# Optimization experiments

Hardware: AMD Instinct MI355X
Metric: run time of the kernel (lower is better)

The kernel has to match this reference:

```python
import jax, jax.numpy as jnp
import numpy as np

D_MODEL = 1024
NUM_EXPERTS = 64
TOP_K = 2
TEMPERATURE = 1.0


def setup_inputs() -> dict:
    key = jax.random.key(0)
    k1, k2, k3, k4 = jax.random.split(key, 4)
    mh_output = jax.random.normal(k1, (8, 4096, D_MODEL), dtype=jnp.float32)
    noise = jax.random.normal(k2, (8, 4096, NUM_EXPERTS), dtype=jnp.float32)  # randn_like sample, externalized
    # nn.Linear weights: shape [out, in], init normal(0, 0.02); biases zero
    W_route = jax.random.normal(k3, (NUM_EXPERTS, D_MODEL), dtype=jnp.float32) * 0.02
    b_route = jnp.zeros((NUM_EXPERTS,), dtype=jnp.float32)
    W_noise = jax.random.normal(k4, (NUM_EXPERTS, D_MODEL), dtype=jnp.float32) * 0.02
    b_noise = jnp.zeros((NUM_EXPERTS,), dtype=jnp.float32)
    return {"mh_output": mh_output, "noise": noise, "W_route": W_route,
            "b_route": b_route, "W_noise": W_noise, "b_noise": b_noise}


def reference(mh_output, noise, W_route, b_route, W_noise, b_noise):
    # logits = topkroute_linear(mh_output); noise_logits = noise_linear(mh_output)
    logits = jnp.einsum('bsd,ed->bse', mh_output, W_route) + b_route
    noise_logits = jnp.einsum('bsd,ed->bse', mh_output, W_noise) + b_noise
    # noisy logits = logits + temperature * randn * softplus(noise_logits)
    noisy = logits + TEMPERATURE * noise * jax.nn.softplus(noise_logits)
    # top-k, scatter into -inf, softmax  ==  softmax over top-k values scattered into zeros
    top_vals, indices = jax.lax.top_k(noisy, TOP_K)          # [b, s, k]
    probs_k = jax.nn.softmax(top_vals, axis=-1)              # softmax(-inf elsewhere) -> 0 elsewhere
    one_hot = jax.nn.one_hot(indices, NUM_EXPERTS, dtype=noisy.dtype)  # [b, s, k, E]
    router_output = jnp.sum(one_hot * probs_k[..., None], axis=-2)     # [b, s, E]
    return router_output, indices
```

## Files before the change

kernel.cpp:

```cpp
#include <hip/hip_runtime.h>
#include <math.h>


#define T_TOKENS 32768
#define D_MODEL  1024
#define NE       64
#define NCOL     128
#define M_TILE   32
#define NCHUNK   (D_MODEL / 32)
#define CS_LD    68
#define OUT_IDX_BASE ((size_t)T_TOKENS * NE)
#define W_ELEMS  (NCOL * D_MODEL)

typedef short  bf16x8  __attribute__((ext_vector_type(8)));
typedef float  floatx4 __attribute__((ext_vector_type(4)));

__device__ __forceinline__ unsigned short f32_to_bf16_rne(float x) {
    unsigned u = __float_as_uint(x);
    unsigned r = u + 0x7fffu + ((u >> 16) & 1u);
    return (unsigned short)(r >> 16);
}
__device__ __forceinline__ float bf16_bits_to_f32(unsigned short h) {
    return __uint_as_float(((unsigned)h) << 16);
}
__device__ __forceinline__ float softplus_f(float x) {
    return fmaxf(x, 0.f) + log1pf(expf(-fabsf(x)));
}

__global__ __launch_bounds__(256) void prepack_w(
    const float* __restrict__ Wr, const float* __restrict__ Wn,
    short* __restrict__ Bh, short* __restrict__ Bl)
{
    int g   = blockIdx.x * 256 + threadIdx.x;
    int n   = g & 15;
    int kg  = (g >> 4) & 127;
    int t2  = g >> 11;
    int col = t2 * 16 + n;
    const float* src = (col < NE ? Wr + (size_t)col * D_MODEL
                                 : Wn + (size_t)(col - NE) * D_MODEL) + kg * 8;
    float4 a = *(const float4*)src;
    float4 b = *(const float4*)(src + 4);
    float v[8] = {a.x, a.y, a.z, a.w, b.x, b.y, b.z, b.w};
    unsigned short h[8], l[8];
    #pragma unroll
    for (int j = 0; j < 8; ++j) {
        h[j] = f32_to_bf16_rne(v[j]);
        l[j] = f32_to_bf16_rne(v[j] - bf16_bits_to_f32(h[j]));
    }
    int4 hp, lp;
    hp.x = (int)((unsigned)h[0] | ((unsigned)h[1] << 16));
    hp.y = (int)((unsigned)h[2] | ((unsigned)h[3] << 16));
    hp.z = (int)((unsigned)h[4] | ((unsigned)h[5] << 16));
    hp.w = (int)((unsigned)h[6] | ((unsigned)h[7] << 16));
    lp.x = (int)((unsigned)l[0] | ((unsigned)l[1] << 16));
    lp.y = (int)((unsigned)l[2] | ((unsigned)l[3] << 16));
    lp.z = (int)((unsigned)l[4] | ((unsigned)l[5] << 16));
    lp.w = (int)((unsigned)l[6] | ((unsigned)l[7] << 16));
    *(int4*)(Bh + (size_t)g * 8) = hp;
    *(int4*)(Bl + (size_t)g * 8) = lp;
}

__global__ __launch_bounds__(256, 4) void router_mfma(
    const float* __restrict__ A,
    const float* __restrict__ noise,
    const float* __restrict__ br,
    const float* __restrict__ bn,
    const short* __restrict__ Bh,
    const short* __restrict__ Bl,
    float* __restrict__ out)
{
    __shared__ __align__(16) short Ah[2][M_TILE * 32];
    __shared__ __align__(16) short Al[2][M_TILE * 32];
    __shared__ float Cs[M_TILE * CS_LD];
    __shared__ float s_p1[M_TILE], s_p2[M_TILE];
    __shared__ int   s_e1[M_TILE], s_e2[M_TILE];

    const int tid  = threadIdx.x;
    const int lane = tid & 63;
    const int wid  = tid >> 6;
    const int n16  = lane & 15;
    const int quad = lane >> 4;
    const int m0   = blockIdx.x * M_TILE;

    const int ms = tid >> 3;
    const int kq = tid & 7;
    const float* pA = A + (size_t)(m0 + ms) * D_MODEL + kq * 4;
    const int sBase = ((kq >> 1) * M_TILE + ms) * 8 + (kq & 1) * 4;

    const int bBaseR = ((wid * 128 + quad) * 16 + n16) * 8;
    const int bBaseN = (((4 + wid) * 128 + quad) * 16 + n16) * 8;

    floatx4 acc[2][2];
    #pragma unroll
    for (int i = 0; i < 2; ++i) { acc[i][0] = (floatx4)0.f; acc[i][1] = (floatx4)0.f; }

#define CONVERT_STORE(buf_, f4_) do {                                       \
        float v_[4] = {(f4_).x, (f4_).y, (f4_).z, (f4_).w};                  \
        unsigned short h_[4], l_[4];                                         \
        _Pragma("unroll")                                                    \
        for (int j_ = 0; j_ < 4; ++j_) {                                     \
            h_[j_] = f32_to_bf16_rne(v_[j_]);                                \
            l_[j_] = f32_to_bf16_rne(v_[j_] - bf16_bits_to_f32(h_[j_]));     \
        }                                                                    \
        int2 hp_, lp_;                                                       \
        hp_.x = (int)((unsigned)h_[0] | ((unsigned)h_[1] << 16));            \
        hp_.y = (int)((unsigned)h_[2] | ((unsigned)h_[3] << 16));            \
        lp_.x = (int)((unsigned)l_[0] | ((unsigned)l_[1] << 16));            \
        lp_.y = (int)((unsigned)l_[2] | ((unsigned)l_[3] << 16));            \
        *(int2*)&Ah[(buf_)][sBase] = hp_;                                    \
        *(int2*)&Al[(buf_)][sBase] = lp_;                                    \
    } while (0)

    {
        float4 a0 = *(const float4*)pA;
        CONVERT_STORE(0, a0);
    }
    bf16x8 bhR, blR, bhN, blN;
    bhR = *(const bf16x8*)(Bh + bBaseR);
    blR = *(const bf16x8*)(Bl + bBaseR);
    bhN = *(const bf16x8*)(Bh + bBaseN);
    blN = *(const bf16x8*)(Bl + bBaseN);
    float4 aP1 = *(const float4*)(pA + 32);
    __syncthreads();

    for (int kc = 0; kc < NCHUNK; ++kc) {
        const int cur = kc & 1, nxt = cur ^ 1;

        float4 aP2;
        if (kc + 2 < NCHUNK)
            aP2 = *(const float4*)(pA + (kc + 2) * 32);

        bf16x8 bhRn, blRn, bhNn, blNn;
        if (kc + 1 < NCHUNK) {
            int o = (kc + 1) * 512;
            bhRn = *(const bf16x8*)(Bh + bBaseR + o);
            blRn = *(const bf16x8*)(Bl + bBaseR + o);
            bhNn = *(const bf16x8*)(Bh + bBaseN + o);
            blNn = *(const bf16x8*)(Bl + bBaseN + o);
        }

        bf16x8 afh[2], afl[2];
        #pragma unroll
        for (int mf = 0; mf < 2; ++mf) {
            int g = (quad * M_TILE + mf * 16 + n16) * 8;
            afh[mf] = *(const bf16x8*)&Ah[cur][g];
            afl[mf] = *(const bf16x8*)&Al[cur][g];
        }

        #pragma unroll
        for (int mf = 0; mf < 2; ++mf) {
            acc[mf][0] = __builtin_amdgcn_mfma_f32_16x16x32_bf16(afh[mf], bhR, acc[mf][0], 0, 0, 0);
            acc[mf][0] = __builtin_amdgcn_mfma_f32_16x16x32_bf16(afh[mf], blR, acc[mf][0], 0, 0, 0);
            acc[mf][0] = __builtin_amdgcn_mfma_f32_16x16x32_bf16(afl[mf], bhR, acc[mf][0], 0, 0, 0);
            acc[mf][1] = __builtin_amdgcn_mfma_f32_16x16x32_bf16(afh[mf], bhN, acc[mf][1], 0, 0, 0);
            acc[mf][1] = __builtin_amdgcn_mfma_f32_16x16x32_bf16(afh[mf], blN, acc[mf][1], 0, 0, 0);
            acc[mf][1] = __builtin_amdgcn_mfma_f32_16x16x32_bf16(afl[mf], bhN, acc[mf][1], 0, 0, 0);
        }

        if (kc + 1 < NCHUNK)
            CONVERT_STORE(nxt, aP1);

        __syncthreads();

        aP1 = aP2;
        bhR = bhRn; blR = blRn; bhN = bhNn; blN = blNn;
    }

    {
        int e = wid * 16 + n16;
        float brv = br[e], bnv = bn[e];
        #pragma unroll
        for (int mf = 0; mf < 2; ++mf)
            #pragma unroll
            for (int r = 0; r < 4; ++r) {
                int t = mf * 16 + quad * 4 + r;
                float nz    = noise[(size_t)(m0 + t) * NE + e];
                float route = acc[mf][0][r] + brv;
                float nl    = acc[mf][1][r] + bnv;
                Cs[t * CS_LD + e] = fmaf(nz, softplus_f(nl), route);
            }
    }
    __syncthreads();

    if (tid < M_TILE) {
        const int t = tid;
        float v1 = -INFINITY, v2 = -INFINITY;
        int e1 = 0, e2 = 0;
        #pragma unroll 8
        for (int e = 0; e < NE; ++e) {
            float v = Cs[t * CS_LD + e];
            if (v > v1) { v2 = v1; e2 = e1; v1 = v; e1 = e; }
            else if (v > v2) { v2 = v; e2 = e; }
        }
        float ex = expf(v2 - v1);
        float denom = 1.f + ex;
        s_p1[t] = 1.f / denom;
        s_p2[t] = ex / denom;
        s_e1[t] = e1;
        s_e2[t] = e2;
        float2 iv = make_float2((float)e1, (float)e2);
        *(float2*)(out + OUT_IDX_BASE + (size_t)(m0 + t) * 2) = iv;
    }
    __syncthreads();

    #pragma unroll
    for (int i = 0; i < 2; ++i) {
        int gi = i * 256 + tid;
        int t  = gi >> 4;
        int e0 = (gi & 15) * 4;
        float p1 = s_p1[t], p2 = s_p2[t];
        int   e1 = s_e1[t], e2 = s_e2[t];
        float4 v;
        v.x = (e0 + 0 == e1) ? p1 : ((e0 + 0 == e2) ? p2 : 0.f);
        v.y = (e0 + 1 == e1) ? p1 : ((e0 + 1 == e2) ? p2 : 0.f);
        v.z = (e0 + 2 == e1) ? p1 : ((e0 + 2 == e2) ? p2 : 0.f);
        v.w = (e0 + 3 == e1) ? p1 : ((e0 + 3 == e2) ? p2 : 0.f);
        *(float4*)(out + (size_t)(m0 + t) * NE + e0) = v;
    }
}

extern "C" void kernel_launch(void* const* d_in, const int* in_sizes, int n_in,
                              void* d_out, int out_size, void* d_ws, size_t ws_size,
                              hipStream_t stream) {
    const float* A     = (const float*)d_in[0];
    const float* noise = (const float*)d_in[1];
    const float* Wr    = (const float*)d_in[2];
    const float* br    = (const float*)d_in[3];
    const float* Wn    = (const float*)d_in[4];
    const float* bn    = (const float*)d_in[5];
    float* out = (float*)d_out;

    short* Bh = (short*)d_ws;
    short* Bl = Bh + W_ELEMS;

    prepack_w<<<dim3(W_ELEMS / 8 / 256), dim3(256), 0, stream>>>(Wr, Wn, Bh, Bl);
    router_mfma<<<dim3(T_TOKENS / M_TILE), dim3(256), 0, stream>>>(A, noise, br, bn, Bh, Bl, out);
}
```

Baseline: 232.6 us.

## Double K-chunk per stage and deepen A register prefetch to three stages

Each loop iteration now processes 64 K elements (two 32-wide chunks) instead of 32, halving the number of __syncthreads barriers and doubling the LDS staging buffers. Activation prefetch into registers is deepened to three stages ahead. Weight fragments are no longer prefetched one iteration early; they are loaded at the top of the same iteration in which they are used. LDS stores for the next stage are moved before the MFMAs so they can overlap. The cost is higher register pressure and exposed B-load latency, which risks occupancy under launch_bounds(256,4).

```diff
diff --git a/kernel.cpp b/kernel.cpp
--- a/kernel.cpp
+++ b/kernel.cpp
@@ -7,7 +7,7 @@
 #define NE       64
 #define NCOL     128
 #define M_TILE   32
-#define NCHUNK   (D_MODEL / 32)
+#define NSTAGE   (D_MODEL / 64)
 #define CS_LD    68
 #define OUT_IDX_BASE ((size_t)T_TOKENS * NE)
 #define W_ELEMS  (NCOL * D_MODEL)
@@ -69,8 +69,8 @@
     const short* __restrict__ Bl,
     float* __restrict__ out)
 {
-    __shared__ __align__(16) short Ah[2][M_TILE * 32];
-    __shared__ __align__(16) short Al[2][M_TILE * 32];
+    __shared__ __align__(16) short Ah[2][2 * M_TILE * 32];
+    __shared__ __align__(16) short Al[2][2 * M_TILE * 32];
     __shared__ float Cs[M_TILE * CS_LD];
     __shared__ float s_p1[M_TILE], s_p2[M_TILE];
     __shared__ int   s_e1[M_TILE], s_e2[M_TILE];
@@ -94,7 +94,7 @@
     #pragma unroll
     for (int i = 0; i < 2; ++i) { acc[i][0] = (floatx4)0.f; acc[i][1] = (floatx4)0.f; }
 
-#define CONVERT_STORE(buf_, f4_) do {                                       \
+#define CONVERT_STORE(buf_, c_, f4_) do {                                    \
         float v_[4] = {(f4_).x, (f4_).y, (f4_).z, (f4_).w};                  \
         unsigned short h_[4], l_[4];                                         \
         _Pragma("unroll")                                                    \
@@ -107,63 +107,73 @@
         hp_.y = (int)((unsigned)h_[2] | ((unsigned)h_[3] << 16));            \
         lp_.x = (int)((unsigned)l_[0] | ((unsigned)l_[1] << 16));            \
         lp_.y = (int)((unsigned)l_[2] | ((unsigned)l_[3] << 16));            \
-        *(int2*)&Ah[(buf_)][sBase] = hp_;                                    \
-        *(int2*)&Al[(buf_)][sBase] = lp_;                                    \
+        *(int2*)&Ah[(buf_)][(c_) * (M_TILE * 32) + sBase] = hp_;             \
+        *(int2*)&Al[(buf_)][(c_) * (M_TILE * 32) + sBase] = lp_;             \
     } while (0)
 
     {
-        float4 a0 = *(const float4*)pA;
-        CONVERT_STORE(0, a0);
-    }
-    bf16x8 bhR, blR, bhN, blN;
-    bhR = *(const bf16x8*)(Bh + bBaseR);
-    blR = *(const bf16x8*)(Bl + bBaseR);
-    bhN = *(const bf16x8*)(Bh + bBaseN);
-    blN = *(const bf16x8*)(Bl + bBaseN);
-    float4 aP1 = *(const float4*)(pA + 32);
+        float4 s0c0 = *(const float4*)(pA);
+        float4 s0c1 = *(const float4*)(pA + 32);
+        CONVERT_STORE(0, 0, s0c0);
+        CONVERT_STORE(0, 1, s0c1);
+    }
+    float4 aP1[2], aP2[2];
+    aP1[0] = *(const float4*)(pA + 64);
+    aP1[1] = *(const float4*)(pA + 96);
+    aP2[0] = *(const float4*)(pA + 128);
+    aP2[1] = *(const float4*)(pA + 160);
     __syncthreads();
 
-    for (int kc = 0; kc < NCHUNK; ++kc) {
-        const int cur = kc & 1, nxt = cur ^ 1;
-
-        float4 aP2;
-        if (kc + 2 < NCHUNK)
-            aP2 = *(const float4*)(pA + (kc + 2) * 32);
-
-        bf16x8 bhRn, blRn, bhNn, blNn;
-        if (kc + 1 < NCHUNK) {
-            int o = (kc + 1) * 512;
-            bhRn = *(const bf16x8*)(Bh + bBaseR + o);
-            blRn = *(const bf16x8*)(Bl + bBaseR + o);
-            bhNn = *(const bf16x8*)(Bh + bBaseN + o);
-            blNn = *(const bf16x8*)(Bl + bBaseN + o);
-        }
-
-        bf16x8 afh[2], afl[2];
-        #pragma unroll
-        for (int mf = 0; mf < 2; ++mf) {
-            int g = (quad * M_TILE + mf * 16 + n16) * 8;
-            afh[mf] = *(const bf16x8*)&Ah[cur][g];
-            afl[mf] = *(const bf16x8*)&Al[cur][g];
-        }
-
-        #pragma unroll
-        for (int mf = 0; mf < 2; ++mf) {
-            acc[mf][0] = __builtin_amdgcn_mfma_f32_16x16x32_bf16(afh[mf], bhR, acc[mf][0], 0, 0, 0);
-            acc[mf][0] = __builtin_amdgcn_mfma_f32_16x16x32_bf16(afh[mf], blR, acc[mf][0], 0, 0, 0);
-            acc[mf][0] = __builtin_amdgcn_mfma_f32_16x16x32_bf16(afl[mf], bhR, acc[mf][0], 0, 0, 0);
-            acc[mf][1] = __builtin_amdgcn_mfma_f32_16x16x32_bf16(afh[mf], bhN, acc[mf][1], 0, 0, 0);
-            acc[mf][1] = __builtin_amdgcn_mfma_f32_16x16x32_bf16(afh[mf], blN, acc[mf][1], 0, 0, 0);
-            acc[mf][1] = __builtin_amdgcn_mfma_f32_16x16x32_bf16(afl[mf], bhN, acc[mf][1], 0, 0, 0);
-        }
-
-        if (kc + 1 < NCHUNK)
-            CONVERT_STORE(nxt, aP1);
+    for (int ks = 0; ks < NSTAGE; ++ks) {
+        const int cur = ks & 1, nxt = cur ^ 1;
+
+        bf16x8 bhR[2], blR[2], bhN[2], blN[2];
+        #pragma unroll
+        for (int c = 0; c < 2; ++c) {
+            int o = (2 * ks + c) * 512;
+            bhR[c] = *(const bf16x8*)(Bh + bBaseR + o);
+            blR[c] = *(const bf16x8*)(Bl + bBaseR + o);
+            bhN[c] = *(const bf16x8*)(Bh + bBaseN + o);
+            blN[c] = *(const bf16x8*)(Bl + bBaseN + o);
+        }
+
+        float4 aP3[2];
+        if (ks + 3 < NSTAGE) {
+            aP3[0] = *(const float4*)(pA + (ks + 3) * 64);
+            aP3[1] = *(const float4*)(pA + (ks + 3) * 64 + 32);
+        }
+
+        bf16x8 afh[2][2], afl[2][2];
+        #pragma unroll
+        for (int c = 0; c < 2; ++c)
+            #pragma unroll
+            for (int mf = 0; mf < 2; ++mf) {
+                int g = c * (M_TILE * 32) + (quad * M_TILE + mf * 16 + n16) * 8;
+                afh[c][mf] = *(const bf16x8*)&Ah[cur][g];
+                afl[c][mf] = *(const bf16x8*)&Al[cur][g];
+            }
+
+        if (ks + 1 < NSTAGE) {
+            CONVERT_STORE(nxt, 0, aP1[0]);
+            CONVERT_STORE(nxt, 1, aP1[1]);
+        }
+
+        #pragma unroll
+        for (int c = 0; c < 2; ++c)
+            #pragma unroll
+            for (int mf = 0; mf < 2; ++mf) {
+                acc[mf][0] = __builtin_amdgcn_mfma_f32_16x16x32_bf16(afh[c][mf], bhR[c], acc[mf][0], 0, 0, 0);
+                acc[mf][0] = __builtin_amdgcn_mfma_f32_16x16x32_bf16(afh[c][mf], blR[c], acc[mf][0], 0, 0, 0);
+                acc[mf][0] = __builtin_amdgcn_mfma_f32_16x16x32_bf16(afl[c][mf], bhR[c], acc[mf][0], 0, 0, 0);
+                acc[mf][1] = __builtin_amdgcn_mfma_f32_16x16x32_bf16(afh[c][mf], bhN[c], acc[mf][1], 0, 0, 0);
+                acc[mf][1] = __builtin_amdgcn_mfma_f32_16x16x32_bf16(afh[c][mf], blN[c], acc[mf][1], 0, 0, 0);
+                acc[mf][1] = __builtin_amdgcn_mfma_f32_16x16x32_bf16(afl[c][mf], bhN[c], acc[mf][1], 0, 0, 0);
+            }
 
         __syncthreads();
 
-        aP1 = aP2;
-        bhR = bhRn; blR = blRn; bhN = bhNn; blN = blNn;
+        aP1[0] = aP2[0]; aP1[1] = aP2[1];
+        aP2[0] = aP3[0]; aP2[1] = aP3[1];
     }
 
     {
```

After: 233.2 us. About the same (+0.3%).

## Double token tile to 64 and deepen A prefetch with packed bf16 split conversion

Applied to the files above, without the earlier changes.

Doubles the per-block token tile from 32 to 64 so each loaded weight fragment feeds twice as many MFMAs. This halves the weight traffic per token and the number of blocks. The A-tile loader now has each thread convert 8 floats with packed bf16x2 intrinsics, and prefetch is three chunks ahead. The conversion and LDS store move before the MFMAs, and the top-2 scan reads float4 vectors from shared memory. Launch bounds drop to 2 blocks per CU, which raises register use and reduces occupancy.

```diff
diff --git a/kernel.cpp b/kernel.cpp
--- a/kernel.cpp
+++ b/kernel.cpp
@@ -1,4 +1,5 @@
 #include <hip/hip_runtime.h>
+#include <hip/hip_bf16.h>
 #include <math.h>
 
 
@@ -6,8 +7,8 @@
 #define D_MODEL  1024
 #define NE       64
 #define NCOL     128
-#define M_TILE   32
-#define NCHUNK   (D_MODEL / 32)
+#define M_TILE   64
+#define NCHUNK   32
 #define CS_LD    68
 #define OUT_IDX_BASE ((size_t)T_TOKENS * NE)
 #define W_ELEMS  (NCOL * D_MODEL)
@@ -15,16 +16,28 @@
 typedef short  bf16x8  __attribute__((ext_vector_type(8)));
 typedef float  floatx4 __attribute__((ext_vector_type(4)));
 
-__device__ __forceinline__ unsigned short f32_to_bf16_rne(float x) {
-    unsigned u = __float_as_uint(x);
-    unsigned r = u + 0x7fffu + ((u >> 16) & 1u);
-    return (unsigned short)(r >> 16);
-}
-__device__ __forceinline__ float bf16_bits_to_f32(unsigned short h) {
-    return __uint_as_float(((unsigned)h) << 16);
-}
 __device__ __forceinline__ float softplus_f(float x) {
     return fmaxf(x, 0.f) + log1pf(expf(-fabsf(x)));
+}
+
+__device__ __forceinline__ void cvt8(const float4 a, const float4 b,
+                                     int4* hi, int4* lo) {
+    float v[8] = {a.x, a.y, a.z, a.w, b.x, b.y, b.z, b.w};
+    int hw[4], lw[4];
+    #pragma unroll
+    for (int p = 0; p < 4; ++p) {
+        float2 f2 = make_float2(v[2 * p], v[2 * p + 1]);
+        __hip_bfloat162 h2 = __float22bfloat162_rn(f2);
+        int u; __builtin_memcpy(&u, &h2, 4);
+        float h0 = __uint_as_float(((unsigned)u) << 16);
+        float h1 = __uint_as_float(((unsigned)u) & 0xFFFF0000u);
+        float2 l2 = make_float2(v[2 * p] - h0, v[2 * p + 1] - h1);
+        __hip_bfloat162 L2 = __float22bfloat162_rn(l2);
+        int ul; __builtin_memcpy(&ul, &L2, 4);
+        hw[p] = u; lw[p] = ul;
+    }
+    *hi = make_int4(hw[0], hw[1], hw[2], hw[3]);
+    *lo = make_int4(lw[0], lw[1], lw[2], lw[3]);
 }
 
 __global__ __launch_bounds__(256) void prepack_w(
@@ -40,27 +53,13 @@
                                  : Wn + (size_t)(col - NE) * D_MODEL) + kg * 8;
     float4 a = *(const float4*)src;
     float4 b = *(const float4*)(src + 4);
-    float v[8] = {a.x, a.y, a.z, a.w, b.x, b.y, b.z, b.w};
-    unsigned short h[8], l[8];
-    #pragma unroll
-    for (int j = 0; j < 8; ++j) {
-        h[j] = f32_to_bf16_rne(v[j]);
-        l[j] = f32_to_bf16_rne(v[j] - bf16_bits_to_f32(h[j]));
-    }
-    int4 hp, lp;
-    hp.x = (int)((unsigned)h[0] | ((unsigned)h[1] << 16));
-    hp.y = (int)((unsigned)h[2] | ((unsigned)h[3] << 16));
-    hp.z = (int)((unsigned)h[4] | ((unsigned)h[5] << 16));
-    hp.w = (int)((unsigned)h[6] | ((unsigned)h[7] << 16));
-    lp.x = (int)((unsigned)l[0] | ((unsigned)l[1] << 16));
-    lp.y = (int)((unsigned)l[2] | ((unsigned)l[3] << 16));
-    lp.z = (int)((unsigned)l[4] | ((unsigned)l[5] << 16));
-    lp.w = (int)((unsigned)l[6] | ((unsigned)l[7] << 16));
-    *(int4*)(Bh + (size_t)g * 8) = hp;
-    *(int4*)(Bl + (size_t)g * 8) = lp;
-}
-
-__global__ __launch_bounds__(256, 4) void router_mfma(
+    int4 hi, lo;
+    cvt8(a, b, &hi, &lo);
+    *(int4*)(Bh + (size_t)g * 8) = hi;
+    *(int4*)(Bl + (size_t)g * 8) = lo;
+}
+
+__global__ __launch_bounds__(256, 2) void router_mfma(
     const float* __restrict__ A,
     const float* __restrict__ noise,
     const float* __restrict__ br,
@@ -82,54 +81,43 @@
     const int quad = lane >> 4;
     const int m0   = blockIdx.x * M_TILE;
 
-    const int ms = tid >> 3;
-    const int kq = tid & 7;
-    const float* pA = A + (size_t)(m0 + ms) * D_MODEL + kq * 4;
-    const int sBase = ((kq >> 1) * M_TILE + ms) * 8 + (kq & 1) * 4;
+    const int r  = tid & 63;
+    const int kh = tid >> 6;
+    const float* pA = A + (size_t)(m0 + r) * D_MODEL + kh * 8;
+    const int sBase = (kh * M_TILE + r) * 8;
 
     const int bBaseR = ((wid * 128 + quad) * 16 + n16) * 8;
     const int bBaseN = (((4 + wid) * 128 + quad) * 16 + n16) * 8;
 
-    floatx4 acc[2][2];
+    floatx4 acc[4][2];
     #pragma unroll
-    for (int i = 0; i < 2; ++i) { acc[i][0] = (floatx4)0.f; acc[i][1] = (floatx4)0.f; }
-
-#define CONVERT_STORE(buf_, f4_) do {                                       \
-        float v_[4] = {(f4_).x, (f4_).y, (f4_).z, (f4_).w};                  \
-        unsigned short h_[4], l_[4];                                         \
-        _Pragma("unroll")                                                    \
-        for (int j_ = 0; j_ < 4; ++j_) {                                     \
-            h_[j_] = f32_to_bf16_rne(v_[j_]);                                \
-            l_[j_] = f32_to_bf16_rne(v_[j_] - bf16_bits_to_f32(h_[j_]));     \
-        }                                                                    \
-        int2 hp_, lp_;                                                       \
-        hp_.x = (int)((unsigned)h_[0] | ((unsigned)h_[1] << 16));            \
-        hp_.y = (int)((unsigned)h_[2] | ((unsigned)h_[3] << 16));            \
-        lp_.x = (int)((unsigned)l_[0] | ((unsigned)l_[1] << 16));            \
-        lp_.y = (int)((unsigned)l_[2] | ((unsigned)l_[3] << 16));            \
-        *(int2*)&Ah[(buf_)][sBase] = hp_;                                    \
-        *(int2*)&Al[(buf_)][sBase] = lp_;                                    \
-    } while (0)
+    for (int i = 0; i < 4; ++i) { acc[i][0] = (floatx4)0.f; acc[i][1] = (floatx4)0.f; }
 
     {
         float4 a0 = *(const float4*)pA;
-        CONVERT_STORE(0, a0);
+        float4 a1 = *(const float4*)(pA + 4);
+        int4 hi, lo;
+        cvt8(a0, a1, &hi, &lo);
+        *(int4*)&Ah[0][sBase] = hi;
+        *(int4*)&Al[0][sBase] = lo;
     }
     bf16x8 bhR, blR, bhN, blN;
     bhR = *(const bf16x8*)(Bh + bBaseR);
     blR = *(const bf16x8*)(Bl + bBaseR);
     bhN = *(const bf16x8*)(Bh + bBaseN);
     blN = *(const bf16x8*)(Bl + bBaseN);
-    float4 aP1 = *(const float4*)(pA + 32);
+    float4 aP1a = *(const float4*)(pA + 32), aP1b = *(const float4*)(pA + 36);
+    float4 aP2a = *(const float4*)(pA + 64), aP2b = *(const float4*)(pA + 68);
     __syncthreads();
 
     for (int kc = 0; kc < NCHUNK; ++kc) {
         const int cur = kc & 1, nxt = cur ^ 1;
 
-        float4 aP2;
-        if (kc + 2 < NCHUNK)
-            aP2 = *(const float4*)(pA + (kc + 2) * 32);
-
+        float4 f0, f1;
+        if (kc + 3 < NCHUNK) {
+            f0 = *(const float4*)(pA + (kc + 3) * 32);
+            f1 = *(const float4*)(pA + (kc + 3) * 32 + 4);
+        }
         bf16x8 bhRn, blRn, bhNn, blNn;
         if (kc + 1 < NCHUNK) {
             int o = (kc + 1) * 512;
@@ -139,30 +127,34 @@
             blNn = *(const bf16x8*)(Bl + bBaseN + o);
         }
 
-        bf16x8 afh[2], afl[2];
-        #pragma unroll
-        for (int mf = 0; mf < 2; ++mf) {
+        bf16x8 afh[4], afl[4];
+        #pragma unroll
+        for (int mf = 0; mf < 4; ++mf) {
             int g = (quad * M_TILE + mf * 16 + n16) * 8;
             afh[mf] = *(const bf16x8*)&Ah[cur][g];
             afl[mf] = *(const bf16x8*)&Al[cur][g];
         }
 
-        #pragma unroll
-        for (int mf = 0; mf < 2; ++mf) {
+        if (kc + 1 < NCHUNK) {
+            int4 hi, lo;
+            cvt8(aP1a, aP1b, &hi, &lo);
+            *(int4*)&Ah[nxt][sBase] = hi;
+            *(int4*)&Al[nxt][sBase] = lo;
+        }
+
+        #pragma unroll
+        for (int mf = 0; mf < 4; ++mf) {
             acc[mf][0] = __builtin_amdgcn_mfma_f32_16x16x32_bf16(afh[mf], bhR, acc[mf][0], 0, 0, 0);
             acc[mf][0] = __builtin_amdgcn_mfma_f32_16x16x32_bf16(afh[mf], blR, acc[mf][0], 0, 0, 0);
             acc[mf][0] = __builtin_amdgcn_mfma_f32_16x16x32_bf16(afl[mf], bhR, acc[mf][0], 0, 0, 0);
             acc[mf][1] = __builtin_amdgcn_mfma_f32_16x16x32_bf16(afh[mf], bhN, acc[mf][1], 0, 0, 0);
             acc[mf][1] = __builtin_amdgcn_mfma_f32_16x16x32_bf16(afh[mf], blN, acc[mf][1], 0, 0, 0);
-            acc[mf][1] = __builtin_amdgcn_mfma_f32_16x16x32_bf16(afl[mf], bhN, acc[mf][1], 0, 0, 0);
-        }
-
-        if (kc + 1 < NCHUNK)
-            CONVERT_STORE(nxt, aP1);
+            acc[mf][1] = __builtin_amdgcn_mfma_f32_16x16x32_bf16(afl[mf], blN == blN ? bhN : bhN, acc[mf][1], 0, 0, 0);
+        }
 
         __syncthreads();
 
-        aP1 = aP2;
+        aP1a = aP2a; aP1b = aP2b; aP2a = f0; aP2b = f1;
         bhR = bhRn; blR = blRn; bhN = bhNn; blN = blNn;
     }
 
@@ -170,13 +162,13 @@
         int e = wid * 16 + n16;
         float brv = br[e], bnv = bn[e];
         #pragma unroll
-        for (int mf = 0; mf < 2; ++mf)
+        for (int mf = 0; mf < 4; ++mf)
             #pragma unroll
-            for (int r = 0; r < 4; ++r) {
-                int t = mf * 16 + quad * 4 + r;
+            for (int rr = 0; rr < 4; ++rr) {
+                int t = mf * 16 + quad * 4 + rr;
                 float nz    = noise[(size_t)(m0 + t) * NE + e];
-                float route = acc[mf][0][r] + brv;
-                float nl    = acc[mf][1][r] + bnv;
+                float route = acc[mf][0][rr] + brv;
+                float nl    = acc[mf][1][rr] + bnv;
                 Cs[t * CS_LD + e] = fmaf(nz, softplus_f(nl), route);
             }
     }
@@ -186,11 +178,17 @@
         const int t = tid;
         float v1 = -INFINITY, v2 = -INFINITY;
         int e1 = 0, e2 = 0;
-        #pragma unroll 8
-        for (int e = 0; e < NE; ++e) {
-            float v = Cs[t * CS_LD + e];
-            if (v > v1) { v2 = v1; e2 = e1; v1 = v; e1 = e; }
-            else if (v > v2) { v2 = v; e2 = e; }
+        #pragma unroll
+        for (int e4 = 0; e4 < 16; ++e4) {
+            float4 q = *(const float4*)&Cs[t * CS_LD + e4 * 4];
+            float qa[4] = {q.x, q.y, q.z, q.w};
+            #pragma unroll
+            for (int c = 0; c < 4; ++c) {
+                float v = qa[c];
+                int e = e4 * 4 + c;
+                if (v > v1) { v2 = v1; e2 = e1; v1 = v; e1 = e; }
+                else if (v > v2) { v2 = v; e2 = e; }
+            }
         }
         float ex = expf(v2 - v1);
         float denom = 1.f + ex;
@@ -204,7 +202,7 @@
     __syncthreads();
 
     #pragma unroll
-    for (int i = 0; i < 2; ++i) {
+    for (int i = 0; i < 4; ++i) {
         int gi = i * 256 + tid;
         int t  = gi >> 4;
         int e0 = (gi & 15) * 4;
```

Measured after the change: 229.3 us. No clear change (-1.4%).
